# Kernel optimization log

Hardware: AMD Instinct MI355X
Metric: run time of the kernel (lower is better)

Reference implementation:

```python
import jax, jax.numpy as jnp
import numpy as np

B, T, H, N = 1, 256, 32, 128
HN = H * N
KVH = 8
KV_DIM = KVH * N
KV_REPEAT = HN // KV_DIM
ROPE_THETA = 10000.0
EPS = 1e-6
NTK_ALPHA = 10.0
YARN_MAX = 4096.0
LORA_W, LORA_A, LORA_V, LORA_G = 64, 64, 32, 128
LAYER_ID = 1


def t5_rmsnorm(x, w):
    xf = x.astype(jnp.float32)
    var = jnp.mean(xf * xf, axis=-1, keepdims=True)
    return (w * (xf * jax.lax.rsqrt(var + EPS))).astype(x.dtype)


def rotate_half(x):
    h = x.shape[-1] // 2
    return jnp.concatenate([-x[..., h:], x[..., :h]], axis=-1)


def rope_cache(cache_pos, seq_len, rotary_dim):
    # YaRN-style mix of short/long inv_freq, per compute_rope_cache_range
    half = rotary_dim // 2
    fs = jnp.arange(half, dtype=jnp.float32)
    inv_short = 1.0 / ROPE_THETA ** (fs / half)
    inv_long = 1.0 / (ROPE_THETA * NTK_ALPHA ** (fs / half))
    pos = cache_pos.astype(jnp.float32) + jnp.arange(seq_len, dtype=jnp.float32)[None, :]  # [B,T]
    mix = jnp.clip(pos / YARN_MAX, 0.0, 1.0)[..., None]
    freqs = (1.0 - mix) * (pos[..., None] * inv_short) + mix * (pos[..., None] * inv_long)
    emb = jnp.concatenate([freqs, freqs], axis=-1)  # [B,T,rotary_dim]
    return jnp.cos(emb), jnp.sin(emb)


def _forward(x_in, v_first, state, cache_position, w0, w1, w2, a0, a1, a2, v0, v1, v2, g1, g2,
             r_k, R_, K_, V_, O_, R_bias, K_bias, V_bias, ln_r, ln_k, ln1, ln2):
    x = t5_rmsnorm(x_in, ln1)  # [B,T,HN]
    # float path of fpx_matmul: x @ W.T (+ bias), i.e. the dequantized math
    r = x @ R_.T + R_bias
    k = x @ K_.T + K_bias
    v = x @ V_.T + V_bias
    r = t5_rmsnorm(r.reshape(B, T, H, N), ln_r)      # [B,T,H,N]
    k = t5_rmsnorm(k.reshape(B, T, KVH, N), ln_k)    # [B,T,KVH,N]
    cos, sin = rope_cache(cache_position, T, N)      # [B,T,N]
    cos_, sin_ = cos[:, :, None, :], sin[:, :, None, :]
    r = r * cos_ + rotate_half(r) * sin_
    k = k * cos_ + rotate_half(k) * sin_
    # decay lora: w = -softplus(-(tanh(x@w1)@w2 + w0)) - 0.5
    w = jnp.tanh(x @ w1) @ w2 + w0
    w = -jax.nn.softplus(-w) - 0.5
    # GQA repeat_kv: each kv head repeated KV_REPEAT times contiguously
    v = v.reshape(B, T, KVH, N)
    k = jnp.repeat(k, KV_REPEAT, axis=2).reshape(B, T, HN)
    v = jnp.repeat(v, KV_REPEAT, axis=2).reshape(B, T, HN)
    a = jax.nn.sigmoid((x @ a1) @ a2 + a0)
    g = jax.nn.sigmoid(x @ g1) @ g2
    k4 = k.reshape(B, T, H, N)
    kk = (k4 / jnp.maximum(jnp.linalg.norm(k4, axis=-1, keepdims=True), 1e-12)).reshape(B, T, HN)
    k = k * (1.0 - w + a)
    aa = -kk
    bb = kk * a
    if LAYER_ID == 0:
        v_first = v
    else:
        gate = jax.nn.sigmoid((x @ v1) @ v2 + v0)
        v = v + (v_first - v) * gate
    w = -jnp.exp(w.astype(jnp.float32))  # log-decay for the recurrence

    def to_tm(t):  # [B,T,HN] or [B,T,H,N] -> time-major [T,B,H,N]
        return jnp.moveaxis(t.reshape(B, T, H, N), 1, 0)

    rt, wt, kt, vt, at, bt = map(to_tm, (r, w, k, v, aa, bb))

    def step(S, inp):
        # RWKV-7: S = S*diag(exp(w)) + S @ (a b^T) + v k^T ; out = S @ r
        r_t, w_t, k_t, v_t, a_t, b_t = inp
        sa = jnp.einsum('bhij,bhj->bhi', S, a_t)
        S = S * jnp.exp(w_t)[:, :, None, :] + sa[..., None] * b_t[:, :, None, :] + v_t[..., None] * k_t[:, :, None, :]
        return S, jnp.einsum('bhij,bhj->bhi', S, r_t)

    S_final, outs = jax.lax.scan(step, state.astype(jnp.float32), (rt, wt, kt, vt, at, bt))
    xx = jnp.moveaxis(outs, 0, 1).reshape(B, T, HN) * (float(N) ** -0.5)
    bonus = jnp.sum(r.reshape(B, T, H, N) * k.reshape(B, T, H, N) * r_k, axis=-1, keepdims=True) * v.reshape(B, T, H, N)
    xx = xx.astype(r.dtype) + bonus.reshape(B, T, HN)
    x_res = x_in + (xx * g) @ O_.T
    out = t5_rmsnorm(x_res, ln2)
    return out, x[:, -1], S_final, v_first, x_res


def setup_inputs() -> dict:
    key = jax.random.key(0)
    ks = iter(jax.random.split(key, 32))
    rn = lambda *s: jax.random.normal(next(ks), s, dtype=jnp.float32)
    wt = lambda *s: rn(*s) * 0.02
    return dict(
        x_in=rn(B, T, HN),
        v_first=rn(B, T, HN),
        state=jnp.zeros((B, H, N, N), jnp.float32),
        cache_position=jnp.zeros((B, 1), jnp.int32),
        w0=wt(HN), w1=wt(HN, LORA_W), w2=wt(LORA_W, HN),
        a0=wt(HN), a1=wt(HN, LORA_A), a2=wt(LORA_A, HN),
        v0=wt(HN), v1=wt(HN, LORA_V), v2=wt(LORA_V, HN),
        g1=wt(HN, LORA_G), g2=wt(LORA_G, HN),
        r_k=wt(H, N),
        R_=wt(HN, HN), K_=wt(KV_DIM, HN), V_=wt(KV_DIM, HN), O_=wt(HN, HN),
        R_bias=wt(HN), K_bias=wt(KV_DIM), V_bias=wt(KV_DIM),
        ln_r=jnp.ones((N,), jnp.float32), ln_k=jnp.ones((N,), jnp.float32),
        ln1=jnp.ones((HN,), jnp.float32), ln2=jnp.ones((HN,), jnp.float32),
    )


def reference(x_in, v_first, state, cache_position, w0, w1, w2, a0, a1, a2, v0, v1, v2, g1, g2,
              r_k, R_, K_, V_, O_, R_bias, K_bias, V_bias, ln_r, ln_k, ln1, ln2):
    return _forward(x_in, v_first, state, cache_position, w0, w1, w2, a0, a1, a2, v0, v1, v2,
                    g1, g2, r_k, R_, K_, V_, O_, R_bias, K_bias, V_bias, ln_r, ln_k, ln1, ln2)
```

## Files before the change

### kernel.cpp

```cpp
#include <hip/hip_runtime.h>
#include <cstdint>
#include <cstddef>

#define T_ 256
#define HN_ 4096
#define H_ 32
#define N_ 128
#define SR_ 6464

typedef __attribute__((ext_vector_type(8))) short short8;
typedef __attribute__((ext_vector_type(4))) float f32x4;

__device__ __forceinline__ short f2bf(float f) {
    uint32_t u = __builtin_bit_cast(uint32_t, f);
    u = (u + 0x7fffu + ((u >> 16) & 1u)) >> 16;
    return (short)u;
}
__device__ __forceinline__ short f2bfc(float f) {
    return (short)((__builtin_bit_cast(uint32_t, f) + 0x8000u) >> 16);
}
__device__ __forceinline__ short8 cvt8r(float4 lo, float4 hi) {
    short8 v;
    v[0] = f2bfc(lo.x); v[1] = f2bfc(lo.y); v[2] = f2bfc(lo.z); v[3] = f2bfc(lo.w);
    v[4] = f2bfc(hi.x); v[5] = f2bfc(hi.y); v[6] = f2bfc(hi.z); v[7] = f2bfc(hi.w);
    return v;
}
__device__ __forceinline__ f32x4 mfma16(short8 a, short8 b, f32x4 c) {
    return __builtin_amdgcn_mfma_f32_16x16x32_bf16(a, b, c, 0, 0, 0);
}
__device__ __forceinline__ float sigm(float x) { return 1.f / (1.f + expf(-x)); }
__device__ __forceinline__ float splus(float x) { return (x > 20.f) ? x : log1pf(expf(x)); }

__device__ __forceinline__ float bf1(ushort u) {
    return __builtin_bit_cast(float, (uint32_t)u << 16);
}
__device__ __forceinline__ void gload_lds16(const void* g, void* l) {
    __builtin_amdgcn_global_load_lds(
        (const __attribute__((address_space(1))) void*)g,
        (__attribute__((address_space(3))) void*)l, 16, 0, 0);
}

template <int CTRL>
__device__ __forceinline__ float dpp_add(float v) {
    int p = __builtin_amdgcn_mov_dpp(__builtin_bit_cast(int, v), CTRL, 0xF, 0xF, true);
    return v + __builtin_bit_cast(float, p);
}
__device__ __forceinline__ float reduce64(float v) {
    v = dpp_add<0xB1>(v);
    v = dpp_add<0x4E>(v);
    v = dpp_add<0x124>(v);
    v = dpp_add<0x128>(v);
    v = dpp_add<0x142>(v);
    v = dpp_add<0x143>(v);
    int r = __builtin_amdgcn_readlane(__builtin_bit_cast(int, v), 63);
    return __builtin_bit_cast(float, r);
}

__device__ __forceinline__ void gemm_core(
    const ushort* __restrict__ A, const float* __restrict__ Brow,
    int kbeg, float* LB, f32x4 acc[2][2]) {
    const int tid = threadIdx.x, wid = tid >> 6, l = tid & 63;
    const int ar = l & 15, ak = (l >> 4) * 8;
    const int mBase = wid * 32;

    const int p1 = tid, p2 = tid + 512;
    const int r1 = p1 >> 5, c1 = (p1 & 31) ^ (r1 & 7);
    const int r2 = p2 >> 5, c2 = (p2 & 31) ^ (r2 & 7);
    const float* sb1 = Brow + (size_t)r1 * 4096 + kbeg + c1 * 4;
    const float* sb2 = Brow + (size_t)r2 * 4096 + kbeg + c2 * 4;
    float* d1 = LB + wid * 256;
    float* d2 = LB + 2048 + wid * 256;

    const ushort* pa0 = A + (size_t)(mBase + ar) * 4096 + kbeg + ak;
    const ushort* pa1 = pa0 + (size_t)16 * 4096;

    const int rb0 = ar * 128, rb1 = (16 + ar) * 128;
    const int sx = ar & 7;
    const int cb = (l >> 4) * 2;

    short8 Ae[8], Ao[8];

#define STAGEB(s, rb) { \
    gload_lds16(sb1 + (size_t)(s) * 128, d1 + (rb) * 4096); \
    gload_lds16(sb2 + (size_t)(s) * 128, d2 + (rb) * 4096); }

#define LA(B_, s) { \
    B_[0] = *(const short8*)(pa0 + (size_t)(s) * 128);      \
    B_[1] = *(const short8*)(pa1 + (size_t)(s) * 128);      \
    B_[2] = *(const short8*)(pa0 + (size_t)(s) * 128 + 32); \
    B_[3] = *(const short8*)(pa1 + (size_t)(s) * 128 + 32); \
    B_[4] = *(const short8*)(pa0 + (size_t)(s) * 128 + 64); \
    B_[5] = *(const short8*)(pa1 + (size_t)(s) * 128 + 64); \
    B_[6] = *(const short8*)(pa0 + (size_t)(s) * 128 + 96); \
    B_[7] = *(const short8*)(pa1 + (size_t)(s) * 128 + 96); }

#define CKK(kk, B_, Lb_) { \
    const int cc = (kk) * 8 + cb; \
    float4 l0 = *(const float4*)(Lb_ + rb0 + ((cc ^ sx) * 4)); \
    float4 h0 = *(const float4*)(Lb_ + rb0 + (((cc + 1) ^ sx) * 4)); \
    float4 l1 = *(const float4*)(Lb_ + rb1 + ((cc ^ sx) * 4)); \
    float4 h1 = *(const float4*)(Lb_ + rb1 + (((cc + 1) ^ sx) * 4)); \
    short8 b0 = cvt8r(l0, h0), b1 = cvt8r(l1, h1); \
    acc[0][0] = mfma16(B_[2 * (kk)], b0, acc[0][0]); \
    acc[0][1] = mfma16(B_[2 * (kk)], b1, acc[0][1]); \
    acc[1][0] = mfma16(B_[2 * (kk) + 1], b0, acc[1][0]); \
    acc[1][1] = mfma16(B_[2 * (kk) + 1], b1, acc[1][1]); }

#define COMPUTE(rb, B_) { const float* Lb_ = LB + (rb) * 4096; \
    CKK(0, B_, Lb_) CKK(1, B_, Lb_) CKK(2, B_, Lb_) CKK(3, B_, Lb_) }

    STAGEB(0, 0)
    LA(Ae, 0)
    STAGEB(1, 1)

    for (int su = 0; su < 4; su++) {
        const int s0 = su * 2, s1 = su * 2 + 1;
        LA(Ao, (s0 + 1 < 8) ? s0 + 1 : 7)
        STAGEB((s0 + 2 < 8) ? s0 + 2 : 7, (s0 + 2) % 3)
        asm volatile("s_waitcnt vmcnt(12)" ::: "memory");
        __builtin_amdgcn_s_barrier();
        __builtin_amdgcn_sched_barrier(0);
        COMPUTE(s0 % 3, Ae)
        __builtin_amdgcn_s_barrier();

        LA(Ae, (s1 + 1 < 8) ? s1 + 1 : 7)
        STAGEB((s1 + 2 < 8) ? s1 + 2 : 7, (s1 + 2) % 3)
        asm volatile("s_waitcnt vmcnt(12)" ::: "memory");
        __builtin_amdgcn_s_barrier();
        __builtin_amdgcn_sched_barrier(0);
        COMPUTE(s1 % 3, Ao)
        __builtin_amdgcn_s_barrier();
    }
    asm volatile("s_waitcnt vmcnt(0)" ::: "memory");
#undef STAGEB
#undef LA
#undef CKK
#undef COMPUTE
}

__global__ __launch_bounds__(256) void rmsnorm_k(const float* __restrict__ in,
                                                 const float* __restrict__ w,
                                                 float* __restrict__ outF,
                                                 ushort* __restrict__ outB,
                                                 float* __restrict__ lastrow) {
    int t = blockIdx.x, tid = threadIdx.x;
    const float4* in4 = (const float4*)(in + (size_t)t * HN_);
    const float4* w4 = (const float4*)w;
    float4 v[4]; float ss = 0.f;
#pragma unroll
    for (int q = 0; q < 4; q++) {
        v[q] = in4[q * 256 + tid];
        ss += v[q].x * v[q].x + v[q].y * v[q].y + v[q].z * v[q].z + v[q].w * v[q].w;
    }
#pragma unroll
    for (int o = 32; o; o >>= 1) ss += __shfl_down(ss, o);
    __shared__ float red[4];
    if ((tid & 63) == 0) red[tid >> 6] = ss;
    __syncthreads();
    float tot = red[0] + red[1] + red[2] + red[3];
    float sc = rsqrtf(tot * (1.f / HN_) + 1e-6f);
#pragma unroll
    for (int q = 0; q < 4; q++) {
        float4 wv = w4[q * 256 + tid];
        float4 r;
        r.x = wv.x * v[q].x * sc; r.y = wv.y * v[q].y * sc;
        r.z = wv.z * v[q].z * sc; r.w = wv.w * v[q].w * sc;
        int idx = q * 256 + tid;
        if (outF) ((float4*)(outF + (size_t)t * HN_))[idx] = r;
        if (outB) {
            ushort4 b;
            b.x = (ushort)f2bf(r.x); b.y = (ushort)f2bf(r.y);
            b.z = (ushort)f2bf(r.z); b.w = (ushort)f2bf(r.w);
            ((ushort4*)(outB + (size_t)t * HN_))[idx] = b;
        }
        if (lastrow && t == T_ - 1) ((float4*)lastrow)[idx] = r;
    }
}

__global__ __launch_bounds__(512, 2) void gemm_rkvt(
    const ushort* __restrict__ A,
    const float* __restrict__ Rw, const float* __restrict__ Kw,
    const float* __restrict__ Vw, const float* __restrict__ WT,
    float* __restrict__ COMB) {
    __shared__ __align__(16) float LB[12288];
    const int tid = threadIdx.x, wid = tid >> 6, l = tid & 63;
    const int mBase = wid * 32;
    const int nB = blockIdx.x * 32;
    const int kbeg = blockIdx.y * 1024;

    const float* Bp; int brow;
    if (nB < 4096)      { Bp = Rw; brow = nB; }
    else if (nB < 5120) { Bp = Kw; brow = nB - 4096; }
    else if (nB < 6144) { Bp = Vw; brow = nB - 5120; }
    else                { Bp = WT; brow = nB - 6144; }

    f32x4 acc[2][2];
#pragma unroll
    for (int i = 0; i < 2; i++)
#pragma unroll
        for (int j = 0; j < 2; j++) acc[i][j] = f32x4{0.f, 0.f, 0.f, 0.f};

    gemm_core(A, Bp + (size_t)brow * 4096, kbeg, LB, acc);

    const int rl = (l >> 4) * 4, cl = l & 15;
#pragma unroll
    for (int mf = 0; mf < 2; mf++)
#pragma unroll
        for (int nf = 0; nf < 2; nf++)
#pragma unroll
            for (int e = 0; e < 4; e++)
                unsafeAtomicAdd(&COMB[(size_t)(mBase + mf * 16 + rl + e) * SR_ + nB + nf * 16 + cl],
                                acc[mf][nf][e]);
}

__global__ __launch_bounds__(512, 2) void gemm_o(
    const ushort* __restrict__ A,
    const float* __restrict__ B,
    float* __restrict__ C) {
    __shared__ __align__(16) float LB[12288];
    const int tid = threadIdx.x, wid = tid >> 6, l = tid & 63;
    const int mBase = wid * 32;
    const int nB = blockIdx.x * 32;
    const int kbeg = blockIdx.y * 1024;

    f32x4 acc[2][2];
#pragma unroll
    for (int i = 0; i < 2; i++)
#pragma unroll
        for (int j = 0; j < 2; j++) acc[i][j] = f32x4{0.f, 0.f, 0.f, 0.f};

    gemm_core(A, B + (size_t)nB * 4096, kbeg, LB, acc);

    const int rl = (l >> 4) * 4, cl = l & 15;
#pragma unroll
    for (int mf = 0; mf < 2; mf++)
#pragma unroll
        for (int nf = 0; nf < 2; nf++)
#pragma unroll
            for (int e = 0; e < 4; e++)
                unsafeAtomicAdd(&C[(size_t)(mBase + mf * 16 + rl + e) * 4096 + nB + nf * 16 + cl],
                                acc[mf][nf][e]);
}

__global__ __launch_bounds__(512) void gemm_s2(
    const ushort* __restrict__ TCB,
    const float* __restrict__ w2, const float* __restrict__ a2,
    const float* __restrict__ v2, const float* __restrict__ g2,
    const float* __restrict__ w0, const float* __restrict__ a0,
    const float* __restrict__ v0,
    float* __restrict__ WPRE, float* __restrict__ APRE,
    float* __restrict__ VGPRE, float* __restrict__ GARR) {
    const int z = blockIdx.y;
    int Aoff, K; const float* B; const float* bias; float* out;
    if (z == 0)      { Aoff = 0;   K = 64;  B = w2; bias = w0;      out = WPRE; }
    else if (z == 1) { Aoff = 64;  K = 64;  B = a2; bias = a0;      out = APRE; }
    else if (z == 2) { Aoff = 128; K = 32;  B = v2; bias = v0;      out = VGPRE; }
    else             { Aoff = 160; K = 128; B = g2; bias = nullptr; out = GARR; }

    const int tid = threadIdx.x, wid = tid >> 6, l = tid & 63;
    const int ar = l & 15, ak = (l >> 4) * 8;
    const int mBase = wid * 32;
    const int nB = blockIdx.x * 32;

    f32x4 acc[2][2];
#pragma unroll
    for (int i = 0; i < 2; i++)
#pragma unroll
        for (int j = 0; j < 2; j++) acc[i][j] = f32x4{0.f, 0.f, 0.f, 0.f};

    for (int k0 = 0; k0 < K; k0 += 32) {
        const ushort* pA = TCB + (size_t)(mBase + ar) * 320 + Aoff + k0 + ak;
        short8 av0 = *(const short8*)pA;
        short8 av1 = *(const short8*)(pA + (size_t)16 * 320);
        short8 bv0, bv1;
#pragma unroll
        for (int e = 0; e < 8; e++) {
            bv0[e] = f2bfc(B[(size_t)(k0 + ak + e) * 4096 + nB + ar]);
            bv1[e] = f2bfc(B[(size_t)(k0 + ak + e) * 4096 + nB + 16 + ar]);
        }
        acc[0][0] = mfma16(av0, bv0, acc[0][0]);
        acc[0][1] = mfma16(av0, bv1, acc[0][1]);
        acc[1][0] = mfma16(av1, bv0, acc[1][0]);
        acc[1][1] = mfma16(av1, bv1, acc[1][1]);
    }
    const int rl = (l >> 4) * 4, cl = l & 15;
#pragma unroll
    for (int mf = 0; mf < 2; mf++)
#pragma unroll
        for (int nf = 0; nf < 2; nf++) {
            int col = nB + nf * 16 + cl;
            float bv = bias ? bias[col] : 0.f;
#pragma unroll
            for (int e = 0; e < 4; e++)
                out[(size_t)(mBase + mf * 16 + rl + e) * 4096 + col] = acc[mf][nf][e] + bv;
        }
}

__global__ __launch_bounds__(256) void wcat2_k(const float* __restrict__ w1p,
                                               const float* __restrict__ a1p,
                                               const float* __restrict__ v1p,
                                               const float* __restrict__ g1p,
                                               float* __restrict__ WT) {
    const int kb = blockIdx.x * 64, tile = blockIdx.y;
    const float* src; int ldw, jo, nb, W;
    if (tile == 0)      { src = w1p; ldw = 64;  jo = 0;  nb = 0;   W = 64; }
    else if (tile == 1) { src = a1p; ldw = 64;  jo = 0;  nb = 64;  W = 64; }
    else if (tile == 2) { src = v1p; ldw = 32;  jo = 0;  nb = 128; W = 32; }
    else if (tile == 3) { src = g1p; ldw = 128; jo = 0;  nb = 160; W = 64; }
    else                { src = g1p; ldw = 128; jo = 64; nb = 224; W = 64; }
    __shared__ float lds[64][65];
    const int ti = threadIdx.x & 63, wi = threadIdx.x >> 6;
    if (ti < W)
        for (int i = wi; i < 64; i += 4)
            lds[i][ti] = src[(size_t)(kb + i) * ldw + jo + ti];
    __syncthreads();
    for (int i2 = wi; i2 < W; i2 += 4)
        WT[(size_t)(nb + i2) * 4096 + kb + ti] = lds[ti][i2];
}

__global__ __launch_bounds__(256) void init_comb_k(const float* __restrict__ Rb,
                                                   const float* __restrict__ Kb,
                                                   const float* __restrict__ Vb,
                                                   float* __restrict__ COMB) {
    int t = blockIdx.x;
    for (int c = threadIdx.x; c < SR_; c += 256) {
        float b = (c < 4096) ? Rb[c] : (c < 5120) ? Kb[c - 4096]
                : (c < 6144) ? Vb[c - 5120] : 0.f;
        COMB[(size_t)t * SR_ + c] = b;
    }
}

__global__ __launch_bounds__(256) void act_k(const float* __restrict__ COMB,
                                             ushort* __restrict__ TCB) {
    int idx = blockIdx.x * 256 + threadIdx.x;
    if (idx >= 256 * 288) return;
    int t = idx / 288, c = idx % 288;
    float v = COMB[(size_t)t * SR_ + 6144 + c];
    if (c < 64) v = tanhf(v);
    else if (c >= 160) v = sigm(v);
    TCB[t * 320 + c] = (ushort)f2bf(v);
}

__global__ void rope_k(const int* __restrict__ cpos, float* __restrict__ cosT,
                       float* __restrict__ sinT) {
    int idx = blockIdx.x * 256 + threadIdx.x;
    int t = idx >> 6, f = idx & 63;
    float pos = (float)cpos[0] + (float)t;
    float mix = fminf(fmaxf(pos * (1.f / 4096.f), 0.f), 1.f);
    float e = (float)f * (1.f / 64.f);
    float inv_s = exp2f(-13.287712379549449f * e);
    float inv_l = exp2f(-13.287712379549449f - 3.321928094887362f * e);
    float fr = pos * ((1.f - mix) * inv_s + mix * inv_l);
    cosT[idx] = cosf(fr);
    sinT[idx] = sinf(fr);
}

__global__ __launch_bounds__(256) void prep_k(
    const float* __restrict__ COMB, const float* __restrict__ wpre,
    const float* __restrict__ apre, const float* __restrict__ vgpre,
    const float* __restrict__ vfirst, const float* __restrict__ garr,
    const float* __restrict__ cosT, const float* __restrict__ sinT,
    const float* __restrict__ lnr, const float* __restrict__ lnk,
    ushort* __restrict__ SFB) {
    int t = blockIdx.x, tid = threadIdx.x;
    int w = tid >> 6, lane = tid & 63;
    float c = cosT[t * 64 + lane], s = sinT[t * 64 + lane];
    float lr0 = lnr[lane], lr1 = lnr[lane + 64];
    float lk0 = lnk[lane], lk1 = lnk[lane + 64];
    const float* r_raw = COMB;
    const float* k_raw = COMB + 4096;
    const float* v_raw = COMB + 5120;
    for (int hb = 0; hb < 8; hb++) {
        int h = hb * 4 + w;
        int kv = h >> 2;
        float r0 = r_raw[(size_t)t * SR_ + h * 128 + lane];
        float r1 = r_raw[(size_t)t * SR_ + h * 128 + 64 + lane];
        float ssum = r0 * r0 + r1 * r1;
#pragma unroll
        for (int o = 32; o; o >>= 1) ssum += __shfl_xor(ssum, o);
        float sc = rsqrtf(ssum * (1.f / 128.f) + 1e-6f);
        float rn0 = lr0 * r0 * sc, rn1 = lr1 * r1 * sc;
        float rr0 = rn0 * c - rn1 * s;
        float rr1 = rn1 * c + rn0 * s;
        float k0 = k_raw[(size_t)t * SR_ + kv * 128 + lane];
        float k1 = k_raw[(size_t)t * SR_ + kv * 128 + 64 + lane];
        float ks = k0 * k0 + k1 * k1;
#pragma unroll
        for (int o = 32; o; o >>= 1) ks += __shfl_xor(ks, o);
        float ksc = rsqrtf(ks * (1.f / 128.f) + 1e-6f);
        float kn0 = lk0 * k0 * ksc, kn1 = lk1 * k1 * ksc;
        float kr0 = kn0 * c - kn1 * s;
        float kr1 = kn1 * c + kn0 * s;
        float nr = kr0 * kr0 + kr1 * kr1;
#pragma unroll
        for (int o = 32; o; o >>= 1) nr += __shfl_xor(nr, o);
        float inv = 1.f / fmaxf(sqrtf(nr), 1e-12f);
        float kk0 = kr0 * inv, kk1 = kr1 * inv;
        int c0 = h * 128 + lane, c1 = c0 + 64;
        size_t tb = (size_t)t * HN_;

        float wv0 = -splus(-wpre[tb + c0]) - 0.5f;
        float wv1 = -splus(-wpre[tb + c1]) - 0.5f;
        float dec0 = expf(-expf(wv0));
        float dec1 = expf(-expf(wv1));
        float av0 = sigm(apre[tb + c0]);
        float av1 = sigm(apre[tb + c1]);
        float vg0 = sigm(vgpre[tb + c0]);
        float vg1 = sigm(vgpre[tb + c1]);
        float vraw0 = v_raw[(size_t)t * SR_ + kv * 128 + lane];
        float vraw1 = v_raw[(size_t)t * SR_ + kv * 128 + 64 + lane];
        float vf0 = vraw0 + (vfirst[tb + c0] - vraw0) * vg0;
        float vf1 = vraw1 + (vfirst[tb + c1] - vraw1) * vg1;

        ushort* sb = SFB + ((size_t)h * T_ + t) * 1024;
        sb[lane]         = (ushort)f2bf(rr0);
        sb[64 + lane]    = (ushort)f2bf(rr1);
        sb[128 + lane]   = (ushort)f2bf(kr0 * (1.f - wv0 + av0));
        sb[192 + lane]   = (ushort)f2bf(kr1 * (1.f - wv1 + av1));
        sb[256 + lane]   = (ushort)f2bf(vf0);
        sb[320 + lane]   = (ushort)f2bf(vf1);
        sb[384 + lane]   = (ushort)f2bf(-kk0);
        sb[448 + lane]   = (ushort)f2bf(-kk1);
        sb[512 + lane]   = (ushort)f2bf(kk0 * av0);
        sb[576 + lane]   = (ushort)f2bf(kk1 * av1);
        sb[640 + lane]   = (ushort)f2bf(garr[tb + c0]);
        sb[704 + lane]   = (ushort)f2bf(garr[tb + c1]);
        float* sw = (float*)(sb + 768);
        sw[lane]      = dec0;
        sw[64 + lane] = dec1;
    }
}

#define SD_ 8
#define SNB_ 9
__global__ __launch_bounds__(512) void scan_k(
    const float* __restrict__ state_in,
    const ushort* __restrict__ SFB,
    const float* __restrict__ rk,
    ushort* __restrict__ yb, float* __restrict__ Sout) {
    const int h = blockIdx.x, sp = blockIdx.y;
    const int tid = threadIdx.x;
    const int wv = tid >> 6, ln = tid & 63;
    const int i = sp * 8 + wv;
    const int j0 = ln * 2;

    float S0, S1;
    {
        float2 s2 = *(const float2*)(state_in + ((size_t)h * 128 + i) * 128 + j0);
        S0 = s2.x; S1 = s2.y;
    }
    float2 rk2 = *(const float2*)(rk + h * 128 + j0);

    __shared__ __align__(16) ushort lds_s[SNB_][1024];
    __shared__ float ybuf[2][8];
    const ushort* hbase = SFB + (size_t)h * T_ * 1024;

    auto STAGE = [&](int buf, int t) {
        if (tid < 128) {
            const ushort* src = hbase + (size_t)(t & (T_ - 1)) * 1024 + tid * 8;
            gload_lds16(src, &lds_s[buf][wv * 512]);
        }
    };

#pragma unroll
    for (int d = 0; d < SD_; d++) STAGE(d, d);

    float cpPend = 0.f;
    int bc = 0, bs = SD_;
    for (int t = 0; t < T_; t++) {
        if (wv < 2) asm volatile("s_waitcnt vmcnt(7)" ::: "memory");
        __builtin_amdgcn_s_barrier();
        __builtin_amdgcn_sched_barrier(0);
        asm volatile("" ::: "memory");

        STAGE(bs, t + SD_);

        if (wv == 7 && ln < 8 && t > 1) {
            yb[(size_t)(t - 2) * HN_ + h * 128 + sp * 8 + ln] =
                (ushort)f2bf(ybuf[t & 1][ln]);
        }

        if (t > 0) {
            float cr = reduce64(cpPend);
            if (ln == 0) ybuf[(t - 1) & 1][wv] = cr;
        }

        const ushort* L = lds_s[bc];
        uint ur = *(const uint*)(L + j0);
        uint uk = *(const uint*)(L + 128 + j0);
        uint ua = *(const uint*)(L + 384 + j0);
        uint ub = *(const uint*)(L + 512 + j0);
        float r0 = bf1((ushort)ur), r1 = bf1((ushort)(ur >> 16));
        float k0 = bf1((ushort)uk), k1 = bf1((ushort)(uk >> 16));
        float a0 = bf1((ushort)ua), a1 = bf1((ushort)(ua >> 16));
        float b0 = bf1((ushort)ub), b1 = bf1((ushort)(ub >> 16));
        float vi = bf1(L[256 + i]);
        float gv = bf1(L[640 + i]);
        float2 w2 = *(const float2*)((const float*)(L + 768) + j0);

        float sa = fmaf(S0, a0, S1 * a1);
        sa = reduce64(sa);

        S0 = fmaf(vi, k0, fmaf(sa, b0, S0 * w2.x));
        S1 = fmaf(vi, k1, fmaf(sa, b1, S1 * w2.y));

        float od = fmaf(S0, r0, S1 * r1);
        float bd = fmaf(r0 * k0, rk2.x, r1 * k1 * rk2.y);
        cpPend = fmaf(od, 0.08838834764831845f, bd * vi) * gv;

        bc = (bc + 1 == SNB_) ? 0 : bc + 1;
        bs = (bs + 1 == SNB_) ? 0 : bs + 1;
    }

    __builtin_amdgcn_s_barrier();
    {
        float cr = reduce64(cpPend);
        if (ln == 0)
            yb[(size_t)(T_ - 1) * HN_ + h * 128 + i] = (ushort)f2bf(cr);
    }
    if (wv == 7 && ln < 8) {
        yb[(size_t)(T_ - 2) * HN_ + h * 128 + sp * 8 + ln] =
            (ushort)f2bf(ybuf[(T_ - 2) & 1][ln]);
    }

    float* p = Sout + ((size_t)h * 128 + i) * 128 + j0;
    *(float2*)p = make_float2(S0, S1);
}

extern "C" void kernel_launch(void* const* d_in, const int* in_sizes, int n_in,
                              void* d_out, int out_size, void* d_ws, size_t ws_size,
                              hipStream_t stream) {
    const float* x_in   = (const float*)d_in[0];
    const float* vfirst = (const float*)d_in[1];
    const float* state  = (const float*)d_in[2];
    const int*   cpos   = (const int*)d_in[3];
    const float* w0 = (const float*)d_in[4];
    const float* w1 = (const float*)d_in[5];
    const float* w2 = (const float*)d_in[6];
    const float* a0 = (const float*)d_in[7];
    const float* a1 = (const float*)d_in[8];
    const float* a2 = (const float*)d_in[9];
    const float* v0 = (const float*)d_in[10];
    const float* v1 = (const float*)d_in[11];
    const float* v2 = (const float*)d_in[12];
    const float* g1 = (const float*)d_in[13];
    const float* g2 = (const float*)d_in[14];
    const float* r_k = (const float*)d_in[15];
    const float* R_ = (const float*)d_in[16];
    const float* K_ = (const float*)d_in[17];
    const float* V_ = (const float*)d_in[18];
    const float* O_ = (const float*)d_in[19];
    const float* Rb = (const float*)d_in[20];
    const float* Kb = (const float*)d_in[21];
    const float* Vb = (const float*)d_in[22];
    const float* ln_r = (const float*)d_in[23];
    const float* ln_k = (const float*)d_in[24];
    const float* ln1 = (const float*)d_in[25];
    const float* ln2 = (const float*)d_in[26];

    float* ws = (float*)d_ws;
    constexpr size_t OFF_XB   = 0;
    constexpr size_t OFF_COMB = 524288;
    constexpr size_t OFF_WT   = 2179072;
    constexpr size_t OFF_TCB  = 3489792;
    constexpr size_t OFF_WPRE = 3530752;
    constexpr size_t OFF_APRE = 4579328;
    constexpr size_t OFF_VGPRE= 5627904;
    constexpr size_t OFF_G    = 6676480;
    constexpr size_t OFF_COS  = 7725056;
    constexpr size_t OFF_SIN  = 7741440;
    constexpr size_t OFF_SF   = 7757824;
    constexpr size_t OFF_YB   = OFF_XB;

    ushort* XB  = (ushort*)(ws + OFF_XB);
    float* COMB = ws + OFF_COMB;
    float* WT   = ws + OFF_WT;
    ushort* TCB = (ushort*)(ws + OFF_TCB);
    float* WPRE = ws + OFF_WPRE;
    float* APRE = ws + OFF_APRE;
    float* VGPRE= ws + OFF_VGPRE;
    float* GARR = ws + OFF_G;
    float* COST = ws + OFF_COS;
    float* SINT = ws + OFF_SIN;
    ushort* SFB = (ushort*)(ws + OFF_SF);
    ushort* YB  = (ushort*)(ws + OFF_YB);

    float* out = (float*)d_out;
    float* out0  = out;
    float* xlast = out + 1048576;
    float* Sfin  = out + 1052672;
    float* vfout = out + 1576960;
    float* xres  = out + 2625536;

    hipMemcpyAsync(vfout, vfirst, (size_t)1048576 * 4, hipMemcpyDeviceToDevice, stream);
    hipMemcpyAsync(xres, x_in, (size_t)1048576 * 4, hipMemcpyDeviceToDevice, stream);

    rmsnorm_k<<<T_, 256, 0, stream>>>(x_in, ln1, nullptr, XB, xlast);

    wcat2_k<<<dim3(64, 5), 256, 0, stream>>>(w1, a1, v1, g1, WT);
    hipMemsetAsync(WT + (size_t)288 * 4096, 0, (size_t)32 * 4096 * 4, stream);
    init_comb_k<<<T_, 256, 0, stream>>>(Rb, Kb, Vb, COMB);

    gemm_rkvt<<<dim3(202, 4), 512, 0, stream>>>(XB, R_, K_, V_, WT, COMB);

    act_k<<<288, 256, 0, stream>>>(COMB, TCB);

    gemm_s2<<<dim3(128, 4), 512, 0, stream>>>(TCB, w2, a2, v2, g2, w0, a0, v0,
                                              WPRE, APRE, VGPRE, GARR);

    rope_k<<<64, 256, 0, stream>>>(cpos, COST, SINT);

    prep_k<<<T_, 256, 0, stream>>>(COMB, WPRE, APRE, VGPRE, vfirst, GARR,
                                   COST, SINT, ln_r, ln_k, SFB);

    scan_k<<<dim3(32, 16), 512, 0, stream>>>(state, SFB, r_k, YB, Sfin);

    gemm_o<<<dim3(128, 4), 512, 0, stream>>>(YB, O_, xres);

    rmsnorm_k<<<T_, 256, 0, stream>>>(xres, ln2, out0, nullptr, nullptr);
}
```

Measured before the change: 324.2 us.

## Fuse two scan timesteps per iteration with precomputed cross-step coefficients

The recurrent scan now advances two timesteps per iteration. prep_k precomputes the step-pair products (decay times the next step's vectors, and the scalar dot products C1-C4 and the bonus terms) so the inner loop needs only four wave reductions per pair instead of two per step, and it keeps one barrier per pair. The rope kernel is folded into prep_k, which computes cos and sin inline and now launches over pairs of tokens and half the heads. The per-pair staged buffer grows from 2KB to 6KB and several coefficients are stored in fp32, which raises LDS and global traffic and changes rounding compared with stepping one token at a time.

```diff
diff --git a/kernel.cpp b/kernel.cpp
--- a/kernel.cpp
+++ b/kernel.cpp
@@ -341,102 +341,117 @@
     TCB[t * 320 + c] = (ushort)f2bf(v);
 }
 
-__global__ void rope_k(const int* __restrict__ cpos, float* __restrict__ cosT,
-                       float* __restrict__ sinT) {
-    int idx = blockIdx.x * 256 + threadIdx.x;
-    int t = idx >> 6, f = idx & 63;
-    float pos = (float)cpos[0] + (float)t;
-    float mix = fminf(fmaxf(pos * (1.f / 4096.f), 0.f), 1.f);
-    float e = (float)f * (1.f / 64.f);
-    float inv_s = exp2f(-13.287712379549449f * e);
-    float inv_l = exp2f(-13.287712379549449f - 3.321928094887362f * e);
-    float fr = pos * ((1.f - mix) * inv_s + mix * inv_l);
-    cosT[idx] = cosf(fr);
-    sinT[idx] = sinf(fr);
-}
-
 __global__ __launch_bounds__(256) void prep_k(
     const float* __restrict__ COMB, const float* __restrict__ wpre,
     const float* __restrict__ apre, const float* __restrict__ vgpre,
     const float* __restrict__ vfirst, const float* __restrict__ garr,
-    const float* __restrict__ cosT, const float* __restrict__ sinT,
+    const float* __restrict__ rkg, const int* __restrict__ cpos,
     const float* __restrict__ lnr, const float* __restrict__ lnk,
     ushort* __restrict__ SFB) {
-    int t = blockIdx.x, tid = threadIdx.x;
-    int w = tid >> 6, lane = tid & 63;
-    float c = cosT[t * 64 + lane], s = sinT[t * 64 + lane];
+    const int tp = blockIdx.x, hg = blockIdx.y;
+    const int tid = threadIdx.x;
+    const int w = tid >> 6, lane = tid & 63;
+    const int t0 = tp * 2, t1 = t0 + 1;
+
+    float e = (float)lane * (1.f / 64.f);
+    float inv_s = exp2f(-13.287712379549449f * e);
+    float inv_l = exp2f(-13.287712379549449f - 3.321928094887362f * e);
+    float base = (float)cpos[0];
+    float pos0 = base + (float)t0, pos1 = base + (float)t1;
+    float mix0 = fminf(fmaxf(pos0 * (1.f / 4096.f), 0.f), 1.f);
+    float mix1 = fminf(fmaxf(pos1 * (1.f / 4096.f), 0.f), 1.f);
+    float fr0 = pos0 * ((1.f - mix0) * inv_s + mix0 * inv_l);
+    float fr1 = pos1 * ((1.f - mix1) * inv_s + mix1 * inv_l);
+    float cA = cosf(fr0), sA = sinf(fr0);
+    float cB = cosf(fr1), sB = sinf(fr1);
+
     float lr0 = lnr[lane], lr1 = lnr[lane + 64];
     float lk0 = lnk[lane], lk1 = lnk[lane + 64];
-    const float* r_raw = COMB;
-    const float* k_raw = COMB + 4096;
-    const float* v_raw = COMB + 5120;
-    for (int hb = 0; hb < 8; hb++) {
+
+    for (int hb = hg * 4; hb < hg * 4 + 4; hb++) {
         int h = hb * 4 + w;
         int kv = h >> 2;
-        float r0 = r_raw[(size_t)t * SR_ + h * 128 + lane];
-        float r1 = r_raw[(size_t)t * SR_ + h * 128 + 64 + lane];
-        float ssum = r0 * r0 + r1 * r1;
-#pragma unroll
-        for (int o = 32; o; o >>= 1) ssum += __shfl_xor(ssum, o);
-        float sc = rsqrtf(ssum * (1.f / 128.f) + 1e-6f);
-        float rn0 = lr0 * r0 * sc, rn1 = lr1 * r1 * sc;
-        float rr0 = rn0 * c - rn1 * s;
-        float rr1 = rn1 * c + rn0 * s;
-        float k0 = k_raw[(size_t)t * SR_ + kv * 128 + lane];
-        float k1 = k_raw[(size_t)t * SR_ + kv * 128 + 64 + lane];
-        float ks = k0 * k0 + k1 * k1;
-#pragma unroll
-        for (int o = 32; o; o >>= 1) ks += __shfl_xor(ks, o);
-        float ksc = rsqrtf(ks * (1.f / 128.f) + 1e-6f);
-        float kn0 = lk0 * k0 * ksc, kn1 = lk1 * k1 * ksc;
-        float kr0 = kn0 * c - kn1 * s;
-        float kr1 = kn1 * c + kn0 * s;
-        float nr = kr0 * kr0 + kr1 * kr1;
-#pragma unroll
-        for (int o = 32; o; o >>= 1) nr += __shfl_xor(nr, o);
-        float inv = 1.f / fmaxf(sqrtf(nr), 1e-12f);
-        float kk0 = kr0 * inv, kk1 = kr1 * inv;
-        int c0 = h * 128 + lane, c1 = c0 + 64;
-        size_t tb = (size_t)t * HN_;
-
-        float wv0 = -splus(-wpre[tb + c0]) - 0.5f;
-        float wv1 = -splus(-wpre[tb + c1]) - 0.5f;
-        float dec0 = expf(-expf(wv0));
-        float dec1 = expf(-expf(wv1));
-        float av0 = sigm(apre[tb + c0]);
-        float av1 = sigm(apre[tb + c1]);
-        float vg0 = sigm(vgpre[tb + c0]);
-        float vg1 = sigm(vgpre[tb + c1]);
-        float vraw0 = v_raw[(size_t)t * SR_ + kv * 128 + lane];
-        float vraw1 = v_raw[(size_t)t * SR_ + kv * 128 + 64 + lane];
-        float vf0 = vraw0 + (vfirst[tb + c0] - vraw0) * vg0;
-        float vf1 = vraw1 + (vfirst[tb + c1] - vraw1) * vg1;
-
-        ushort* sb = SFB + ((size_t)h * T_ + t) * 1024;
-        sb[lane]         = (ushort)f2bf(rr0);
-        sb[64 + lane]    = (ushort)f2bf(rr1);
-        sb[128 + lane]   = (ushort)f2bf(kr0 * (1.f - wv0 + av0));
-        sb[192 + lane]   = (ushort)f2bf(kr1 * (1.f - wv1 + av1));
-        sb[256 + lane]   = (ushort)f2bf(vf0);
-        sb[320 + lane]   = (ushort)f2bf(vf1);
-        sb[384 + lane]   = (ushort)f2bf(-kk0);
-        sb[448 + lane]   = (ushort)f2bf(-kk1);
-        sb[512 + lane]   = (ushort)f2bf(kk0 * av0);
-        sb[576 + lane]   = (ushort)f2bf(kk1 * av1);
-        sb[640 + lane]   = (ushort)f2bf(garr[tb + c0]);
-        sb[704 + lane]   = (ushort)f2bf(garr[tb + c1]);
-        float* sw = (float*)(sb + 768);
-        sw[lane]      = dec0;
-        sw[64 + lane] = dec1;
-    }
-}
-
-#define SD_ 8
-#define SNB_ 9
+        float rk0 = rkg[h * 128 + lane], rk1 = rkg[h * 128 + 64 + lane];
+
+        auto STEPQ = [&](int t, float cc, float ss,
+                         float& Rr0, float& Rr1, float& Kf0, float& Kf1,
+                         float& Aa0, float& Aa1, float& Bb0, float& Bb1,
+                         float& Dd0, float& Dd1, float& Vv0, float& Vv1,
+                         float& Gg0, float& Gg1) {
+            size_t tS = (size_t)t * SR_;
+            float r0 = COMB[tS + h * 128 + lane];
+            float r1 = COMB[tS + h * 128 + 64 + lane];
+            float sm = reduce64(r0 * r0 + r1 * r1);
+            float sc = rsqrtf(sm * (1.f / 128.f) + 1e-6f);
+            float rn0 = lr0 * r0 * sc, rn1 = lr1 * r1 * sc;
+            Rr0 = rn0 * cc - rn1 * ss; Rr1 = rn1 * cc + rn0 * ss;
+            float k0 = COMB[tS + 4096 + kv * 128 + lane];
+            float k1 = COMB[tS + 4096 + kv * 128 + 64 + lane];
+            float ks = reduce64(k0 * k0 + k1 * k1);
+            float ksc = rsqrtf(ks * (1.f / 128.f) + 1e-6f);
+            float kn0 = lk0 * k0 * ksc, kn1 = lk1 * k1 * ksc;
+            float kr0 = kn0 * cc - kn1 * ss, kr1 = kn1 * cc + kn0 * ss;
+            float nr = reduce64(kr0 * kr0 + kr1 * kr1);
+            float inv = 1.f / fmaxf(sqrtf(nr), 1e-12f);
+            float kk0 = kr0 * inv, kk1 = kr1 * inv;
+            int ch0 = h * 128 + lane, ch1 = ch0 + 64;
+            size_t tb = (size_t)t * HN_;
+            float wv0 = -splus(-wpre[tb + ch0]) - 0.5f;
+            float wv1 = -splus(-wpre[tb + ch1]) - 0.5f;
+            Dd0 = expf(-expf(wv0)); Dd1 = expf(-expf(wv1));
+            float av0 = sigm(apre[tb + ch0]);
+            float av1 = sigm(apre[tb + ch1]);
+            float vg0 = sigm(vgpre[tb + ch0]);
+            float vg1 = sigm(vgpre[tb + ch1]);
+            float vr0 = COMB[tS + 5120 + kv * 128 + lane];
+            float vr1 = COMB[tS + 5120 + kv * 128 + 64 + lane];
+            Vv0 = vr0 + (vfirst[tb + ch0] - vr0) * vg0;
+            Vv1 = vr1 + (vfirst[tb + ch1] - vr1) * vg1;
+            Kf0 = kr0 * (1.f - wv0 + av0); Kf1 = kr1 * (1.f - wv1 + av1);
+            Aa0 = -kk0; Aa1 = -kk1;
+            Bb0 = kk0 * av0; Bb1 = kk1 * av1;
+            Gg0 = garr[tb + ch0]; Gg1 = garr[tb + ch1];
+        };
+
+        float r00, r01, k00, k01, a00, a01, b00, b01, d00, d01, v00, v01, g00, g01;
+        float r10, r11, k10, k11, a10, a11, b10, b11, d10, d11, v10, v11, g10, g11;
+        STEPQ(t0, cA, sA, r00, r01, k00, k01, a00, a01, b00, b01, d00, d01, v00, v01, g00, g01);
+        STEPQ(t1, cB, sB, r10, r11, k10, k11, a10, a11, b10, b11, d10, d11, v10, v11, g10, g11);
+
+        float* rf = (float*)(SFB + ((size_t)h * 128 + tp) * 3072);
+        rf[0    + lane] = a00;        rf[0    + 64 + lane] = a01;
+        rf[128  + lane] = d00 * a10;  rf[128  + 64 + lane] = d01 * a11;
+        rf[256  + lane] = d00 * r00;  rf[256  + 64 + lane] = d01 * r01;
+        rf[384  + lane] = r10;        rf[384  + 64 + lane] = r11;
+        rf[512  + lane] = d00 * d10;  rf[512  + 64 + lane] = d01 * d11;
+        rf[640  + lane] = b00 * d10;  rf[640  + 64 + lane] = b01 * d11;
+        rf[768  + lane] = k00 * d10;  rf[768  + 64 + lane] = k01 * d11;
+        rf[896  + lane] = b10;        rf[896  + 64 + lane] = b11;
+        rf[1024 + lane] = k10;        rf[1024 + 64 + lane] = k11;
+        ushort* us = (ushort*)rf;
+        us[2304 + lane] = (ushort)f2bf(v00); us[2304 + 64 + lane] = (ushort)f2bf(v01);
+        us[2432 + lane] = (ushort)f2bf(v10); us[2432 + 64 + lane] = (ushort)f2bf(v11);
+        us[2560 + lane] = (ushort)f2bf(g00); us[2560 + 64 + lane] = (ushort)f2bf(g01);
+        us[2688 + lane] = (ushort)f2bf(g10); us[2688 + 64 + lane] = (ushort)f2bf(g11);
+
+        float C1  = reduce64(b00 * a10 + b01 * a11);
+        float C2  = reduce64(k00 * a10 + k01 * a11);
+        float C3  = reduce64(b00 * r00 + b01 * r01);
+        float C4  = reduce64(k00 * r00 + k01 * r01);
+        float BD0 = reduce64(r00 * k00 * rk0 + r01 * k01 * rk1);
+        float BD1 = reduce64(r10 * k10 * rk0 + r11 * k11 * rk1);
+        if (lane == 0) {
+            rf[1408] = C1; rf[1409] = C2; rf[1410] = C3;
+            rf[1411] = C4; rf[1412] = BD0; rf[1413] = BD1;
+        }
+    }
+}
+
+#define SDP_ 8
+#define SNBP_ 9
 __global__ __launch_bounds__(512) void scan_k(
     const float* __restrict__ state_in,
     const ushort* __restrict__ SFB,
-    const float* __restrict__ rk,
     ushort* __restrict__ yb, float* __restrict__ Sout) {
     const int h = blockIdx.x, sp = blockIdx.y;
     const int tid = threadIdx.x;
@@ -449,82 +464,108 @@
         float2 s2 = *(const float2*)(state_in + ((size_t)h * 128 + i) * 128 + j0);
         S0 = s2.x; S1 = s2.y;
     }
-    float2 rk2 = *(const float2*)(rk + h * 128 + j0);
-
-    __shared__ __align__(16) ushort lds_s[SNB_][1024];
-    __shared__ float ybuf[2][8];
-    const ushort* hbase = SFB + (size_t)h * T_ * 1024;
-
-    auto STAGE = [&](int buf, int t) {
-        if (tid < 128) {
-            const ushort* src = hbase + (size_t)(t & (T_ - 1)) * 1024 + tid * 8;
+
+    __shared__ __align__(16) ushort lds_s[SNBP_][3072];
+    __shared__ float ybuf[3][16];
+    const ushort* hbase = SFB + (size_t)h * 128 * 3072;
+
+    auto STAGE = [&](int buf, int tp) {
+        if (wv < 6) {
+            const ushort* src = hbase + (size_t)(tp & 127) * 3072 + wv * 512 + ln * 8;
             gload_lds16(src, &lds_s[buf][wv * 512]);
         }
     };
 
 #pragma unroll
-    for (int d = 0; d < SD_; d++) STAGE(d, d);
-
-    float cpPend = 0.f;
-    int bc = 0, bs = SD_;
-    for (int t = 0; t < T_; t++) {
-        if (wv < 2) asm volatile("s_waitcnt vmcnt(7)" ::: "memory");
+    for (int d = 0; d < SDP_; d++) STAGE(d, d);
+
+    float r1c0 = 0.f, r1c1 = 0.f, bd1c = 0.f, vi1c = 0.f, gi1c = 0.f;
+    int bc = 0, bs = SDP_;
+    for (int I = 0; I < 128; I++) {
+        if (wv < 6) asm volatile("s_waitcnt vmcnt(7)" ::: "memory");
         __builtin_amdgcn_s_barrier();
         __builtin_amdgcn_sched_barrier(0);
         asm volatile("" ::: "memory");
 
-        STAGE(bs, t + SD_);
-
-        if (wv == 7 && ln < 8 && t > 1) {
-            yb[(size_t)(t - 2) * HN_ + h * 128 + sp * 8 + ln] =
-                (ushort)f2bf(ybuf[t & 1][ln]);
-        }
-
-        if (t > 0) {
-            float cr = reduce64(cpPend);
-            if (ln == 0) ybuf[(t - 1) & 1][wv] = cr;
+        STAGE(bs, I + SDP_);
+
+        if (wv == 7 && ln < 16 && I > 1) {
+            int pr = I - 2;
+            int row = sp * 8 + (ln >> 1);
+            int tt = pr * 2 + (ln & 1);
+            yb[(size_t)tt * HN_ + h * 128 + row] = (ushort)f2bf(ybuf[pr % 3][ln]);
         }
 
         const ushort* L = lds_s[bc];
-        uint ur = *(const uint*)(L + j0);
-        uint uk = *(const uint*)(L + 128 + j0);
-        uint ua = *(const uint*)(L + 384 + j0);
-        uint ub = *(const uint*)(L + 512 + j0);
-        float r0 = bf1((ushort)ur), r1 = bf1((ushort)(ur >> 16));
-        float k0 = bf1((ushort)uk), k1 = bf1((ushort)(uk >> 16));
-        float a0 = bf1((ushort)ua), a1 = bf1((ushort)(ua >> 16));
-        float b0 = bf1((ushort)ub), b1 = bf1((ushort)(ub >> 16));
-        float vi = bf1(L[256 + i]);
-        float gv = bf1(L[640 + i]);
-        float2 w2 = *(const float2*)((const float*)(L + 768) + j0);
-
-        float sa = fmaf(S0, a0, S1 * a1);
-        sa = reduce64(sa);
-
-        S0 = fmaf(vi, k0, fmaf(sa, b0, S0 * w2.x));
-        S1 = fmaf(vi, k1, fmaf(sa, b1, S1 * w2.y));
-
-        float od = fmaf(S0, r0, S1 * r1);
-        float bd = fmaf(r0 * k0, rk2.x, r1 * k1 * rk2.y);
-        cpPend = fmaf(od, 0.08838834764831845f, bd * vi) * gv;
-
-        bc = (bc + 1 == SNB_) ? 0 : bc + 1;
-        bs = (bs + 1 == SNB_) ? 0 : bs + 1;
+        const float* Lf = (const float*)L;
+        float2 A0 = *(const float2*)(Lf + 0    + j0);
+        float2 WA = *(const float2*)(Lf + 128  + j0);
+        float2 WR = *(const float2*)(Lf + 256  + j0);
+        float2 R1 = *(const float2*)(Lf + 384  + j0);
+        float2 W2 = *(const float2*)(Lf + 512  + j0);
+        float2 BW = *(const float2*)(Lf + 640  + j0);
+        float2 KW = *(const float2*)(Lf + 768  + j0);
+        float2 B1 = *(const float2*)(Lf + 896  + j0);
+        float2 K1 = *(const float2*)(Lf + 1024 + j0);
+        float vi0 = bf1(L[2304 + i]);
+        float vi1 = bf1(L[2432 + i]);
+        float gi0 = bf1(L[2560 + i]);
+        float gi1 = bf1(L[2688 + i]);
+        const float* Sc = Lf + 1408;
+        float c1 = Sc[0], c2 = Sc[1], c3 = Sc[2], c4 = Sc[3];
+        float bd0 = Sc[4], bd1 = Sc[5];
+
+        float up = fmaf(S0, A0.x, S1 * A0.y);
+        float pp = fmaf(S0, WA.x, S1 * WA.y);
+        float yp = fmaf(S0, WR.x, S1 * WR.y);
+        float op = fmaf(S0, r1c0, S1 * r1c1);
+        float u   = reduce64(up);
+        float p   = reduce64(pp);
+        float yb0 = reduce64(yp);
+        float od1 = reduce64(op);
+
+        if (I > 0) {
+            float cp1 = fmaf(od1, 0.08838834764831845f, bd1c * vi1c) * gi1c;
+            if (ln == 0) ybuf[(I - 1) % 3][2 * wv + 1] = cp1;
+        }
+
+        float sa0 = u;
+        float sa1 = fmaf(sa0, c1, fmaf(vi0, c2, p));
+        float od0 = fmaf(sa0, c3, fmaf(vi0, c4, yb0));
+        float cp0 = fmaf(od0, 0.08838834764831845f, bd0 * vi0) * gi0;
+        if (ln == 0) ybuf[I % 3][2 * wv] = cp0;
+
+        S0 = fmaf(sa0, BW.x, S0 * W2.x);
+        S0 = fmaf(vi0, KW.x, S0);
+        S0 = fmaf(sa1, B1.x, S0);
+        S0 = fmaf(vi1, K1.x, S0);
+        S1 = fmaf(sa0, BW.y, S1 * W2.y);
+        S1 = fmaf(vi0, KW.y, S1);
+        S1 = fmaf(sa1, B1.y, S1);
+        S1 = fmaf(vi1, K1.y, S1);
+
+        r1c0 = R1.x; r1c1 = R1.y;
+        bd1c = bd1; vi1c = vi1; gi1c = gi1;
+
+        bc = (bc + 1 == SNBP_) ? 0 : bc + 1;
+        bs = (bs + 1 == SNBP_) ? 0 : bs + 1;
     }
 
     __builtin_amdgcn_s_barrier();
     {
-        float cr = reduce64(cpPend);
-        if (ln == 0)
-            yb[(size_t)(T_ - 1) * HN_ + h * 128 + i] = (ushort)f2bf(cr);
-    }
-    if (wv == 7 && ln < 8) {
-        yb[(size_t)(T_ - 2) * HN_ + h * 128 + sp * 8 + ln] =
-            (ushort)f2bf(ybuf[(T_ - 2) & 1][ln]);
-    }
-
-    float* p = Sout + ((size_t)h * 128 + i) * 128 + j0;
-    *(float2*)p = make_float2(S0, S1);
+        float op = fmaf(S0, r1c0, S1 * r1c1);
+        float od1 = reduce64(op);
+        float cp1 = fmaf(od1, 0.08838834764831845f, bd1c * vi1c) * gi1c;
+        if (ln == 0) {
+            yb[(size_t)255 * HN_ + h * 128 + i] = (ushort)f2bf(cp1);
+            yb[(size_t)254 * HN_ + h * 128 + i] = (ushort)f2bf(ybuf[1][2 * wv]);
+            yb[(size_t)252 * HN_ + h * 128 + i] = (ushort)f2bf(ybuf[0][2 * wv]);
+            yb[(size_t)253 * HN_ + h * 128 + i] = (ushort)f2bf(ybuf[0][2 * wv + 1]);
+        }
+    }
+
+    float* pS = Sout + ((size_t)h * 128 + i) * 128 + j0;
+    *(float2*)pS = make_float2(S0, S1);
 }
 
 extern "C" void kernel_launch(void* const* d_in, const int* in_sizes, int n_in,
@@ -567,8 +608,6 @@
     constexpr size_t OFF_APRE = 4579328;
     constexpr size_t OFF_VGPRE= 5627904;
     constexpr size_t OFF_G    = 6676480;
-    constexpr size_t OFF_COS  = 7725056;
-    constexpr size_t OFF_SIN  = 7741440;
     constexpr size_t OFF_SF   = 7757824;
     constexpr size_t OFF_YB   = OFF_XB;
 
@@ -580,8 +619,6 @@
     float* APRE = ws + OFF_APRE;
     float* VGPRE= ws + OFF_VGPRE;
     float* GARR = ws + OFF_G;
-    float* COST = ws + OFF_COS;
-    float* SINT = ws + OFF_SIN;
     ushort* SFB = (ushort*)(ws + OFF_SF);
     ushort* YB  = (ushort*)(ws + OFF_YB);
 
@@ -608,12 +645,10 @@
     gemm_s2<<<dim3(128, 4), 512, 0, stream>>>(TCB, w2, a2, v2, g2, w0, a0, v0,
                                               WPRE, APRE, VGPRE, GARR);
 
-    rope_k<<<64, 256, 0, stream>>>(cpos, COST, SINT);
-
-    prep_k<<<T_, 256, 0, stream>>>(COMB, WPRE, APRE, VGPRE, vfirst, GARR,
-                                   COST, SINT, ln_r, ln_k, SFB);
-
-    scan_k<<<dim3(32, 16), 512, 0, stream>>>(state, SFB, r_k, YB, Sfin);
+    prep_k<<<dim3(128, 2), 256, 0, stream>>>(COMB, WPRE, APRE, VGPRE, vfirst, GARR,
+                                             r_k, cpos, ln_r, ln_k, SFB);
+
+    scan_k<<<dim3(32, 16), 512, 0, stream>>>(state, SFB, YB, Sfin);
 
     gemm_o<<<dim3(128, 4), 512, 0, stream>>>(YB, O_, xres);
 
```

Result: faster. 314.7 us (-2.9%).
